# Performance work log

Measured on AMD Instinct MI355X. Metric: run time of the kernel, lower is better.

The kernel has to match this reference:

```python
import jax, jax.numpy as jnp
import numpy as np

N_DIM = 1024   # nodes (rows of s, rows of Kweight)
IN_DIM = 1024  # nodes / feature dim (cols of s, rows of Qweight, side of Gmat)
H_DIM = 64
B = 16


def setup_inputs() -> dict:
    key = jax.random.key(0)
    k1, k2, k3, k4 = jax.random.split(key, 4)
    s = jax.random.normal(k1, (N_DIM, B, IN_DIM), dtype=jnp.float32)
    Gmat = jax.random.uniform(k2, (IN_DIM, IN_DIM), dtype=jnp.float32)
    # torch init: rand * (4/d)**0.5 - (1/d)**0.5  => U[-(1/d)**0.5, (1/d)**0.5]... kept faithful
    Qweight = jax.random.uniform(k3, (IN_DIM, H_DIM), dtype=jnp.float32) * (4.0 / IN_DIM) ** 0.5 - (1.0 / IN_DIM) ** 0.5
    Kweight = jax.random.uniform(k4, (N_DIM, H_DIM), dtype=jnp.float32) * (4.0 / N_DIM) ** 0.5 - (1.0 / N_DIM) ** 0.5
    return {"s": s, "Gmat": Gmat, "Qweight": Qweight, "Kweight": Kweight}


def reference(s, Gmat, Qweight, Kweight):
    h_dim = Qweight.shape[1]
    inv_sqrt_h = 1.0 / jnp.sqrt(jnp.float32(h_dim))
    # q: einsum('ijk,km->ijm', s, Qw).permute(1,0,2) -> (B, n, h)
    q = jnp.einsum('nbi,ih->bnh', s, Qweight)
    # k: s.permute(1,2,0) einsum Kw then permute(0,2,1) -> (B, h, i)
    k = jnp.einsum('nbi,nh->bhi', s, Kweight)
    # squared (non-softmax) attention scores: (B, n, i)
    att = jnp.square(jnp.einsum('bnh,bhi->bni', q, k) * inv_sqrt_h + 1e-9)
    # adjacency aggregation: (B, n, i) @ (i, i)
    att = jnp.einsum('bni,ij->bnj', att, Gmat)
    # row-normalize and permute back to (n, B, i)
    s_t = jnp.sum(att, axis=2, keepdims=True) + 0.001
    return (att / s_t).transpose(1, 0, 2)
```

## Files before the change

### kernel.cpp

```cpp
#include <hip/hip_runtime.h>
#include <hip/hip_bf16.h>
#include <stdint.h>

typedef unsigned short u16;
typedef unsigned int   u32;

#define N_DIM  1024
#define IN_DIM 1024
#define H_DIM  64
#define BATCH  16

typedef __bf16 bf16x8 __attribute__((ext_vector_type(8)));
typedef float  f32x4  __attribute__((ext_vector_type(4)));

__device__ inline u16 f2bf(float f) {
    union { float f; u32 u; } v; v.f = f;
    u32 u = v.u;
    return (u16)((u + 0x7fffu + ((u >> 16) & 1u)) >> 16);
}
__device__ inline u32 pack2(float a, float b) {
    __hip_bfloat162 h = __float22bfloat162_rn(float2{a, b});
    union { __hip_bfloat162 h; u32 u; } cv; cv.h = h; return cv.u;
}

__device__ inline void gl_lds16(const u16* g, u16* l) {
    __builtin_amdgcn_global_load_lds(
        (const __attribute__((address_space(1))) u32*)g,
        (__attribute__((address_space(3))) u32*)l, 16, 0, 0);
}

__global__ __launch_bounds__(256) void prep(
        const float* __restrict__ G, const float* __restrict__ Q,
        const float* __restrict__ Kw, u16* __restrict__ Gbt,
        float* __restrict__ Grp, u16* __restrict__ QT, u16* __restrict__ KwT) {
    int bid = blockIdx.x;
    if (bid >= 256) {
        int idx = (bid - 256) * 256 + threadIdx.x;
        const float* src = (idx < 65536) ? Q : Kw;
        u16* dst = (idx < 65536) ? QT : KwT;
        int i = idx & 65535;
        int h = i >> 10;
        int n = i & 1023;
        dst[h * 1024 + n] = f2bf(src[n * 64 + h]);
        return;
    }
    __shared__ float tile[64][65];
    int jt = bid & 15, it = bid >> 4;
    int i0 = it * 64, j0 = jt * 64;
    int tx = threadIdx.x & 63, ty = threadIdx.x >> 6;
    for (int r = 0; r < 16; ++r) {
        int i = ty * 16 + r;
        tile[i][tx] = G[(size_t)(i0 + i) * 1024 + j0 + tx];
    }
    __syncthreads();
    for (int r = 0; r < 16; ++r) {
        int j = ty * 16 + r;
        Gbt[(size_t)(j0 + j) * 1024 + i0 + tx] = f2bf(tile[tx][j]);
    }
    if (ty == 0) {
        float sum = 0.f;
        for (int j = 0; j < 64; ++j) sum += tile[tx][j];
        Grp[jt * 1024 + i0 + tx] = sum;
    }
}

__global__ __launch_bounds__(512, 4) void qkt(
        const float* __restrict__ s, const u16* __restrict__ QT,
        const u16* __restrict__ KwT, const float* __restrict__ Grp,
        u16* __restrict__ qws, u16* __restrict__ ktws, float* __restrict__ Grsum) {
    int b = blockIdx.y;
    int t = threadIdx.x, lane = t & 63, w = t >> 6, quad = lane >> 4, l15 = lane & 15;
    __shared__ __align__(16) u16 sh[2][2][64][34];
    float* red = (float*)sh;

    if (blockIdx.z == 0) {
        if (blockIdx.y == 0 && t < 64) {
            int i = blockIdx.x * 64 + t;
            float g = 0.f;
            for (int jt = 0; jt < 16; ++jt) g += Grp[jt * 1024 + i];
            Grsum[i] = g;
        }
        int n0 = blockIdx.x * 64;
        int wm = (w & 3) * 16;
        int kb = (w >> 2) * 512;
        const float* arow = s + (size_t)(n0 + wm + l15) * (BATCH * IN_DIM)
                              + (size_t)b * IN_DIM + kb + quad * 8;
        const u16* bbase = QT + (size_t)l15 * 1024 + kb + quad * 8;

        f32x4 acc[4] = {};
        float4 A0[3], A1[3];
        bf16x8 Bf[2][4];
        A0[0] = ((const float4*)arow)[0];
        A1[0] = ((const float4*)arow)[1];
        A0[1] = ((const float4*)(arow + 32))[0];
        A1[1] = ((const float4*)(arow + 32))[1];
#pragma unroll
        for (int ct = 0; ct < 4; ++ct)
            Bf[0][ct] = *(const bf16x8*)&bbase[ct * 16384];

#pragma unroll
        for (int st = 0; st < 16; ++st) {
            int cur = st % 3, cb = st & 1;
            if (st < 14) {
                const float4* ap = (const float4*)(arow + (size_t)(st + 2) * 32);
                A0[(st + 2) % 3] = ap[0];
                A1[(st + 2) % 3] = ap[1];
            }
            if (st < 15) {
#pragma unroll
                for (int ct = 0; ct < 4; ++ct)
                    Bf[cb ^ 1][ct] = *(const bf16x8*)&bbase[ct * 16384 + (st + 1) * 32];
            }
            float4 fa = A0[cur], fb = A1[cur];
            union { uint4 u; bf16x8 v; } cu;
            cu.u = (uint4){ pack2(fa.x, fa.y), pack2(fa.z, fa.w),
                            pack2(fb.x, fb.y), pack2(fb.z, fb.w) };
#pragma unroll
            for (int ct = 0; ct < 4; ++ct)
                acc[ct] = __builtin_amdgcn_mfma_f32_16x16x32_bf16(cu.v, Bf[cb][ct], acc[ct], 0, 0, 0);
        }

        if (w >= 4) {
            float* dst = red + ((w - 4) * 64 + lane) * 16;
#pragma unroll
            for (int ct = 0; ct < 4; ++ct) *(f32x4*)&dst[ct * 4] = acc[ct];
        }
        __syncthreads();
        if (w < 4) {
            const float* sp2 = red + (w * 64 + lane) * 16;
            u16* ob = qws + (size_t)b * 65536;
#pragma unroll
            for (int ct = 0; ct < 4; ++ct) {
                f32x4 o = *(const f32x4*)&sp2[ct * 4];
#pragma unroll
                for (int r = 0; r < 4; ++r) {
                    int m = n0 + wm + quad * 4 + r;
                    ob[(size_t)m * 64 + ct * 16 + l15] = f2bf(acc[ct][r] + o[r]);
                }
            }
        }
        return;
    }

    int i0 = blockIdx.x * 64;
    int half = w >> 2;
    int wm = (w & 3) * 16;
    int shalf = t >> 8, nr = (t & 255) >> 3, iofs = (t & 7) * 8;
    const float* sp = s + (size_t)(shalf * 512 + nr) * (BATCH * IN_DIM)
                        + (size_t)b * IN_DIM + i0 + iofs;
    const u16* bbase = KwT + (size_t)l15 * 1024 + half * 512 + quad * 8;

    f32x4 acc[4] = {};
    float4 P0[2], P1[2];
    bf16x8 Bf[2][4];
    P0[0] = ((const float4*)sp)[0];
    P1[0] = ((const float4*)sp)[1];
    {
        const float4* p = (const float4*)(sp + (size_t)32 * 16384);
        P0[1] = p[0]; P1[1] = p[1];
    }
#pragma unroll
    for (int ct = 0; ct < 4; ++ct)
        Bf[0][ct] = *(const bf16x8*)&bbase[ct * 16384];

#pragma unroll
    for (int c = 0; c < 16; ++c) {
        int buf = c & 1;
        float4 fa = P0[buf], fb = P1[buf];
        u16* wp = &sh[shalf][buf][iofs][nr];
        wp[0]   = f2bf(fa.x);
        wp[34]  = f2bf(fa.y);
        wp[68]  = f2bf(fa.z);
        wp[102] = f2bf(fa.w);
        wp[136] = f2bf(fb.x);
        wp[170] = f2bf(fb.y);
        wp[204] = f2bf(fb.z);
        wp[238] = f2bf(fb.w);
        __syncthreads();
        if (c < 14) {
            const float4* p = (const float4*)(sp + (size_t)(c + 2) * 32 * 16384);
            P0[buf] = p[0]; P1[buf] = p[1];
        }
        if (c < 15) {
#pragma unroll
            for (int ct = 0; ct < 4; ++ct)
                Bf[(c + 1) & 1][ct] = *(const bf16x8*)&bbase[ct * 16384 + (c + 1) * 32];
        }
        const u32* ap = (const u32*)&sh[half][buf][wm + l15][quad * 8];
        union { u32 u[4]; bf16x8 v; } au;
        au.u[0] = ap[0]; au.u[1] = ap[1]; au.u[2] = ap[2]; au.u[3] = ap[3];
#pragma unroll
        for (int ct = 0; ct < 4; ++ct)
            acc[ct] = __builtin_amdgcn_mfma_f32_16x16x32_bf16(au.v, Bf[buf][ct], acc[ct], 0, 0, 0);
    }

    __syncthreads();
    if (w >= 4) {
        float* dst = red + ((w - 4) * 64 + lane) * 16;
#pragma unroll
        for (int ct = 0; ct < 4; ++ct) *(f32x4*)&dst[ct * 4] = acc[ct];
    }
    __syncthreads();
    if (w < 4) {
        const float* sp2 = red + (w * 64 + lane) * 16;
        u16* ob = ktws + (size_t)b * 65536;
#pragma unroll
        for (int ct = 0; ct < 4; ++ct) {
            f32x4 o = *(const f32x4*)&sp2[ct * 4];
#pragma unroll
            for (int r = 0; r < 4; ++r) {
                int i = i0 + wm + quad * 4 + r;
                ob[(size_t)i * 64 + ct * 16 + l15] = f2bf(acc[ct][r] + o[r]);
            }
        }
    }
}

__global__ __launch_bounds__(256, 2) void gemm_fused(
        const u16* __restrict__ qws, const u16* __restrict__ ktws,
        const u16* __restrict__ Gbt, const float* __restrict__ Grsum,
        float* __restrict__ out) {
    int b = blockIdx.z;
    int n0 = blockIdx.x * 256, m0 = blockIdx.y * 128;
    const u16* qb = qws  + (size_t)b * 65536;
    const u16* kb = ktws + (size_t)b * 65536;
    __shared__ __align__(16) u16 As[128 * 40];
    __shared__ __align__(16) u16 Bs[2][256 * 32];
    __shared__ __align__(16) u16 ktc[32 * 72];
    __shared__ __align__(16) float Grs[1024];
    __shared__ float rs[128];
    int t = threadIdx.x, lane = t & 63, w = t >> 6, quad = lane >> 4, l15 = lane & 15;
    int ti = w & 1;
    int wm = (w >> 1) * 64;
    int wn = (w & 1) * 128;

    ((float4*)Grs)[t] = ((const float4*)Grsum)[t];
    if (t < 128) rs[t] = 0.f;

    bf16x8 qf[4][2];
    for (int j = 0; j < 4; ++j)
        for (int kick = 0; kick < 2; ++kick)
            qf[j][kick] = *(const bf16x8*)&qb[(size_t)(m0 + wm + j*16 + l15) * 64 + kick*32 + quad*8];

    int br = t >> 2, bc = ((t & 3) ^ (br & 3)) * 8;
    for (int g4 = 0; g4 < 4; ++g4)
        gl_lds16(Gbt + (size_t)(n0 + br + g4*64) * 1024 + bc, &Bs[0][(br + g4*64) * 32 + (t & 3) * 8]);
    int ir = t >> 3, ch = (t & 7) * 8;
    uint4 kreg = *(const uint4*)&kb[(size_t)ir * 64 + ch];
    int khs = (quad ^ (l15 & 3)) * 8;

    f32x4 acc[4][8] = {};
    float partial[4] = {0.f, 0.f, 0.f, 0.f};

    for (int kk = 0; kk < 32; ++kk) {
        int buf = kk & 1;
        *(uint4*)&ktc[ir * 72 + ch] = kreg;
        __syncthreads();
        f32x4 sacc[4] = {};
        for (int kick = 0; kick < 2; ++kick) {
            bf16x8 ktf = *(const bf16x8*)&ktc[(ti*16 + l15) * 72 + kick*32 + quad*8];
            for (int j = 0; j < 4; ++j)
                sacc[j] = __builtin_amdgcn_mfma_f32_16x16x32_bf16(ktf, qf[j][kick], sacc[j], 0, 0, 0);
        }
        if (kk < 31)
            kreg = *(const uint4*)&kb[(size_t)((kk + 1) * 32 + ir) * 64 + ch];
        float4 g = *(const float4*)&Grs[kk * 32 + ti * 16 + quad * 4];
        for (int j = 0; j < 4; ++j) {
            float v0 = sacc[j][0] * 0.125f + 1e-9f; v0 *= v0;
            float v1 = sacc[j][1] * 0.125f + 1e-9f; v1 *= v1;
            float v2 = sacc[j][2] * 0.125f + 1e-9f; v2 *= v2;
            float v3 = sacc[j][3] * 0.125f + 1e-9f; v3 *= v3;
            partial[j] += v0 * g.x + v1 * g.y + v2 * g.z + v3 * g.w;
            uint2 pk = { pack2(v0, v1), pack2(v2, v3) };
            *(uint2*)&As[(wm + j*16 + l15) * 40 + ti*16 + quad*4] = pk;
        }
        __syncthreads();
        if (kk < 31) {
            for (int g4 = 0; g4 < 4; ++g4)
                gl_lds16(Gbt + (size_t)(n0 + br + g4*64) * 1024 + (kk+1)*32 + bc,
                         &Bs[buf^1][(br + g4*64) * 32 + (t & 3) * 8]);
        }
        int kh = quad * 8;
        bf16x8 af[4];
        for (int i = 0; i < 4; ++i) af[i] = *(const bf16x8*)&As[(wm + i*16 + l15) * 40 + kh];
        for (int jh = 0; jh < 2; ++jh) {
            bf16x8 bfr[4];
            for (int j = 0; j < 4; ++j)
                bfr[j] = *(const bf16x8*)&Bs[buf][(wn + jh*64 + j*16 + l15) * 32 + khs];
            for (int i = 0; i < 4; ++i)
                for (int j = 0; j < 4; ++j)
                    acc[i][jh*4 + j] = __builtin_amdgcn_mfma_f32_16x16x32_bf16(af[i], bfr[j], acc[i][jh*4 + j], 0, 0, 0);
        }
    }

    for (int j = 0; j < 4; ++j) {
        partial[j] += __shfl_xor(partial[j], 16, 64);
        partial[j] += __shfl_xor(partial[j], 32, 64);
    }
    if (quad == 0)
        for (int j = 0; j < 4; ++j) atomicAdd(&rs[wm + j*16 + l15], partial[j]);
    __syncthreads();
    if (t < 128) rs[t] = 1.0f / (rs[t] + 0.001f);
    __syncthreads();

    for (int i = 0; i < 4; ++i) {
        float4 rv = *(const float4*)&rs[wm + i * 16 + quad * 4];
        float rva[4] = { rv.x, rv.y, rv.z, rv.w };
        for (int r = 0; r < 4; ++r) {
            int m = m0 + wm + i * 16 + quad * 4 + r;
            float* orow = out + (size_t)m * (BATCH * IN_DIM) + (size_t)b * IN_DIM + n0 + wn;
            for (int j = 0; j < 8; ++j)
                orow[j * 16 + l15] = acc[i][j][r] * rva[r];
        }
    }
}

extern "C" void kernel_launch(void* const* d_in, const int* in_sizes, int n_in,
                              void* d_out, int out_size, void* d_ws, size_t ws_size,
                              hipStream_t stream) {
    const float* s  = (const float*)d_in[0];
    const float* G  = (const float*)d_in[1];
    const float* Q  = (const float*)d_in[2];
    const float* Kw = (const float*)d_in[3];
    float* out = (float*)d_out;
    char* ws = (char*)d_ws;

    u16*   qws   = (u16*)(ws);
    u16*   ktws  = (u16*)(ws + (size_t)(2u << 20));
    u16*   Gbt   = (u16*)(ws + (size_t)(4u << 20));
    u16*   QT    = (u16*)(ws + (size_t)(6u << 20));
    u16*   KwT   = (u16*)(ws + (size_t)(6u << 20) + (128u << 10));
    float* Grsum = (float*)(ws + (size_t)(6u << 20) + (256u << 10));
    float* Grp   = (float*)(ws + (size_t)(6u << 20) + (260u << 10));

    prep<<<768, 256, 0, stream>>>(G, Q, Kw, Gbt, Grp, QT, KwT);
    qkt<<<dim3(16, 16, 2), 512, 0, stream>>>(s, QT, KwT, Grp, qws, ktws, Grsum);
    gemm_fused<<<dim3(4, 8, 16), 256, 0, stream>>>(qws, ktws, Gbt, Grsum, out);
}
```

Before: 197.5 us.

## Give each warp full-width row tiles and compute its scores independently

```diff
diff --git a/kernel.cpp b/kernel.cpp
--- a/kernel.cpp
+++ b/kernel.cpp
@@ -226,91 +226,113 @@
     const u16* kb = ktws + (size_t)b * 65536;
     __shared__ __align__(16) u16 As[128 * 40];
     __shared__ __align__(16) u16 Bs[2][256 * 32];
-    __shared__ __align__(16) u16 ktc[32 * 72];
     __shared__ __align__(16) float Grs[1024];
-    __shared__ float rs[128];
+    __shared__ float rsw[128];
     int t = threadIdx.x, lane = t & 63, w = t >> 6, quad = lane >> 4, l15 = lane & 15;
-    int ti = w & 1;
-    int wm = (w >> 1) * 64;
-    int wn = (w & 1) * 128;
+    int wm = w * 32;
 
     ((float4*)Grs)[t] = ((const float4*)Grsum)[t];
-    if (t < 128) rs[t] = 0.f;
-
-    bf16x8 qf[4][2];
-    for (int j = 0; j < 4; ++j)
+
+    bf16x8 qf[2][2];
+#pragma unroll
+    for (int jm = 0; jm < 2; ++jm)
+#pragma unroll
         for (int kick = 0; kick < 2; ++kick)
-            qf[j][kick] = *(const bf16x8*)&qb[(size_t)(m0 + wm + j*16 + l15) * 64 + kick*32 + quad*8];
-
-    int br = t >> 2, bc = ((t & 3) ^ (br & 3)) * 8;
+            qf[jm][kick] = *(const bf16x8*)&qb[(size_t)(m0 + wm + jm*16 + l15) * 64 + kick*32 + quad*8];
+
+    int br = t >> 2, bc = (t & 3) * 8;
+#pragma unroll
     for (int g4 = 0; g4 < 4; ++g4)
-        gl_lds16(Gbt + (size_t)(n0 + br + g4*64) * 1024 + bc, &Bs[0][(br + g4*64) * 32 + (t & 3) * 8]);
-    int ir = t >> 3, ch = (t & 7) * 8;
-    uint4 kreg = *(const uint4*)&kb[(size_t)ir * 64 + ch];
-    int khs = (quad ^ (l15 & 3)) * 8;
-
-    f32x4 acc[4][8] = {};
-    float partial[4] = {0.f, 0.f, 0.f, 0.f};
+        gl_lds16(Gbt + (size_t)(n0 + br + g4*64) * 1024 + bc, &Bs[0][(br + g4*64) * 32 + bc]);
+
+    bf16x8 kc[2][2], kn[2][2];
+#pragma unroll
+    for (int it = 0; it < 2; ++it)
+#pragma unroll
+        for (int kick = 0; kick < 2; ++kick)
+            kc[it][kick] = *(const bf16x8*)&kb[(size_t)(it*16 + l15) * 64 + kick*32 + quad*8];
+
+    f32x4 acc[2][16] = {};
+    float partial[2] = {0.f, 0.f};
 
     for (int kk = 0; kk < 32; ++kk) {
         int buf = kk & 1;
-        *(uint4*)&ktc[ir * 72 + ch] = kreg;
-        __syncthreads();
-        f32x4 sacc[4] = {};
-        for (int kick = 0; kick < 2; ++kick) {
-            bf16x8 ktf = *(const bf16x8*)&ktc[(ti*16 + l15) * 72 + kick*32 + quad*8];
-            for (int j = 0; j < 4; ++j)
-                sacc[j] = __builtin_amdgcn_mfma_f32_16x16x32_bf16(ktf, qf[j][kick], sacc[j], 0, 0, 0);
-        }
-        if (kk < 31)
-            kreg = *(const uint4*)&kb[(size_t)((kk + 1) * 32 + ir) * 64 + ch];
-        float4 g = *(const float4*)&Grs[kk * 32 + ti * 16 + quad * 4];
-        for (int j = 0; j < 4; ++j) {
-            float v0 = sacc[j][0] * 0.125f + 1e-9f; v0 *= v0;
-            float v1 = sacc[j][1] * 0.125f + 1e-9f; v1 *= v1;
-            float v2 = sacc[j][2] * 0.125f + 1e-9f; v2 *= v2;
-            float v3 = sacc[j][3] * 0.125f + 1e-9f; v3 *= v3;
-            partial[j] += v0 * g.x + v1 * g.y + v2 * g.z + v3 * g.w;
-            uint2 pk = { pack2(v0, v1), pack2(v2, v3) };
-            *(uint2*)&As[(wm + j*16 + l15) * 40 + ti*16 + quad*4] = pk;
-        }
         __syncthreads();
         if (kk < 31) {
+#pragma unroll
             for (int g4 = 0; g4 < 4; ++g4)
                 gl_lds16(Gbt + (size_t)(n0 + br + g4*64) * 1024 + (kk+1)*32 + bc,
-                         &Bs[buf^1][(br + g4*64) * 32 + (t & 3) * 8]);
-        }
-        int kh = quad * 8;
-        bf16x8 af[4];
-        for (int i = 0; i < 4; ++i) af[i] = *(const bf16x8*)&As[(wm + i*16 + l15) * 40 + kh];
-        for (int jh = 0; jh < 2; ++jh) {
-            bf16x8 bfr[4];
-            for (int j = 0; j < 4; ++j)
-                bfr[j] = *(const bf16x8*)&Bs[buf][(wn + jh*64 + j*16 + l15) * 32 + khs];
-            for (int i = 0; i < 4; ++i)
-                for (int j = 0; j < 4; ++j)
-                    acc[i][jh*4 + j] = __builtin_amdgcn_mfma_f32_16x16x32_bf16(af[i], bfr[j], acc[i][jh*4 + j], 0, 0, 0);
-        }
-    }
-
-    for (int j = 0; j < 4; ++j) {
-        partial[j] += __shfl_xor(partial[j], 16, 64);
-        partial[j] += __shfl_xor(partial[j], 32, 64);
+                         &Bs[buf^1][(br + g4*64) * 32 + bc]);
+        }
+        f32x4 sacc[2][2] = {};
+#pragma unroll
+        for (int kick = 0; kick < 2; ++kick)
+#pragma unroll
+            for (int it = 0; it < 2; ++it)
+#pragma unroll
+                for (int jm = 0; jm < 2; ++jm)
+                    sacc[it][jm] = __builtin_amdgcn_mfma_f32_16x16x32_bf16(
+                        kc[it][kick], qf[jm][kick], sacc[it][jm], 0, 0, 0);
+        if (kk < 31) {
+#pragma unroll
+            for (int it = 0; it < 2; ++it)
+#pragma unroll
+                for (int kick = 0; kick < 2; ++kick)
+                    kn[it][kick] = *(const bf16x8*)&kb[(size_t)((kk+1)*32 + it*16 + l15) * 64 + kick*32 + quad*8];
+        }
+#pragma unroll
+        for (int it = 0; it < 2; ++it) {
+            float4 g = *(const float4*)&Grs[kk * 32 + it * 16 + quad * 4];
+#pragma unroll
+            for (int jm = 0; jm < 2; ++jm) {
+                float v0 = sacc[it][jm][0] * 0.125f + 1e-9f; v0 *= v0;
+                float v1 = sacc[it][jm][1] * 0.125f + 1e-9f; v1 *= v1;
+                float v2 = sacc[it][jm][2] * 0.125f + 1e-9f; v2 *= v2;
+                float v3 = sacc[it][jm][3] * 0.125f + 1e-9f; v3 *= v3;
+                partial[jm] += v0 * g.x + v1 * g.y + v2 * g.z + v3 * g.w;
+                uint2 pk = { pack2(v0, v1), pack2(v2, v3) };
+                *(uint2*)&As[(wm + jm*16 + l15) * 40 + it*16 + quad*4] = pk;
+            }
+        }
+        bf16x8 af[2];
+#pragma unroll
+        for (int mf = 0; mf < 2; ++mf)
+            af[mf] = *(const bf16x8*)&As[(wm + mf*16 + l15) * 40 + quad*8];
+#pragma unroll
+        for (int nf = 0; nf < 16; ++nf) {
+            bf16x8 bfr = *(const bf16x8*)&Bs[buf][(nf*16 + l15) * 32 + quad*8];
+#pragma unroll
+            for (int mf = 0; mf < 2; ++mf)
+                acc[mf][nf] = __builtin_amdgcn_mfma_f32_16x16x32_bf16(af[mf], bfr, acc[mf][nf], 0, 0, 0);
+        }
+#pragma unroll
+        for (int it = 0; it < 2; ++it)
+#pragma unroll
+            for (int kick = 0; kick < 2; ++kick)
+                kc[it][kick] = kn[it][kick];
+    }
+
+#pragma unroll
+    for (int jm = 0; jm < 2; ++jm) {
+        partial[jm] += __shfl_xor(partial[jm], 16, 64);
+        partial[jm] += __shfl_xor(partial[jm], 32, 64);
     }
     if (quad == 0)
-        for (int j = 0; j < 4; ++j) atomicAdd(&rs[wm + j*16 + l15], partial[j]);
-    __syncthreads();
-    if (t < 128) rs[t] = 1.0f / (rs[t] + 0.001f);
-    __syncthreads();
-
-    for (int i = 0; i < 4; ++i) {
-        float4 rv = *(const float4*)&rs[wm + i * 16 + quad * 4];
+#pragma unroll
+        for (int jm = 0; jm < 2; ++jm)
+            rsw[wm + jm*16 + l15] = 1.0f / (partial[jm] + 0.001f);
+
+#pragma unroll
+    for (int mf = 0; mf < 2; ++mf) {
+        float4 rv = *(const float4*)&rsw[wm + mf * 16 + quad * 4];
         float rva[4] = { rv.x, rv.y, rv.z, rv.w };
+#pragma unroll
         for (int r = 0; r < 4; ++r) {
-            int m = m0 + wm + i * 16 + quad * 4 + r;
-            float* orow = out + (size_t)m * (BATCH * IN_DIM) + (size_t)b * IN_DIM + n0 + wn;
-            for (int j = 0; j < 8; ++j)
-                orow[j * 16 + l15] = acc[i][j][r] * rva[r];
+            int m = m0 + wm + mf * 16 + quad * 4 + r;
+            float* orow = out + (size_t)m * (BATCH * IN_DIM) + (size_t)b * IN_DIM + n0;
+#pragma unroll
+            for (int nf = 0; nf < 16; ++nf)
+                orow[nf * 16 + l15] = acc[mf][nf][r] * rva[r];
         }
     }
 }
```

Result: slower. 207.3 us (+5.0%).

## Retile fused GEMM to 64x256 blocks with direct-from-global operand fragments

Applied to the files above, without the earlier changes.

```diff
diff --git a/kernel.cpp b/kernel.cpp
--- a/kernel.cpp
+++ b/kernel.cpp
@@ -21,12 +21,6 @@
 __device__ inline u32 pack2(float a, float b) {
     __hip_bfloat162 h = __float22bfloat162_rn(float2{a, b});
     union { __hip_bfloat162 h; u32 u; } cv; cv.h = h; return cv.u;
-}
-
-__device__ inline void gl_lds16(const u16* g, u16* l) {
-    __builtin_amdgcn_global_load_lds(
-        (const __attribute__((address_space(1))) u32*)g,
-        (__attribute__((address_space(3))) u32*)l, 16, 0, 0);
 }
 
 __global__ __launch_bounds__(256) void prep(
@@ -216,101 +210,87 @@
     }
 }
 
-__global__ __launch_bounds__(256, 2) void gemm_fused(
+__global__ __launch_bounds__(512, 4) void gemm_fused(
         const u16* __restrict__ qws, const u16* __restrict__ ktws,
         const u16* __restrict__ Gbt, const float* __restrict__ Grsum,
         float* __restrict__ out) {
     int b = blockIdx.z;
-    int n0 = blockIdx.x * 256, m0 = blockIdx.y * 128;
+    int n0 = blockIdx.x * 256, m0 = blockIdx.y * 64;
     const u16* qb = qws  + (size_t)b * 65536;
     const u16* kb = ktws + (size_t)b * 65536;
-    __shared__ __align__(16) u16 As[128 * 40];
-    __shared__ __align__(16) u16 Bs[2][256 * 32];
-    __shared__ __align__(16) u16 ktc[32 * 72];
-    __shared__ __align__(16) float Grs[1024];
-    __shared__ float rs[128];
+    __shared__ __align__(16) u16 As[2][64 * 40];
+    __shared__ float rs[64];
     int t = threadIdx.x, lane = t & 63, w = t >> 6, quad = lane >> 4, l15 = lane & 15;
     int ti = w & 1;
-    int wm = (w >> 1) * 64;
-    int wn = (w & 1) * 128;
-
-    ((float4*)Grs)[t] = ((const float4*)Grsum)[t];
-    if (t < 128) rs[t] = 0.f;
-
-    bf16x8 qf[4][2];
-    for (int j = 0; j < 4; ++j)
-        for (int kick = 0; kick < 2; ++kick)
-            qf[j][kick] = *(const bf16x8*)&qb[(size_t)(m0 + wm + j*16 + l15) * 64 + kick*32 + quad*8];
-
-    int br = t >> 2, bc = ((t & 3) ^ (br & 3)) * 8;
-    for (int g4 = 0; g4 < 4; ++g4)
-        gl_lds16(Gbt + (size_t)(n0 + br + g4*64) * 1024 + bc, &Bs[0][(br + g4*64) * 32 + (t & 3) * 8]);
-    int ir = t >> 3, ch = (t & 7) * 8;
-    uint4 kreg = *(const uint4*)&kb[(size_t)ir * 64 + ch];
-    int khs = (quad ^ (l15 & 3)) * 8;
-
-    f32x4 acc[4][8] = {};
-    float partial[4] = {0.f, 0.f, 0.f, 0.f};
+    int sm = (w >> 1) * 16;
+    int wn = w * 32;
+
+    if (t < 64) rs[t] = 0.f;
+
+    bf16x8 qf[2];
+#pragma unroll
+    for (int kick = 0; kick < 2; ++kick)
+        qf[kick] = *(const bf16x8*)&qb[(size_t)(m0 + sm + l15) * 64 + kick*32 + quad*8];
+
+    bf16x8 kc[2], kn[2];
+#pragma unroll
+    for (int kick = 0; kick < 2; ++kick)
+        kc[kick] = *(const bf16x8*)&kb[(size_t)(ti*16 + l15) * 64 + kick*32 + quad*8];
+
+    f32x4 acc[4][2] = {};
+    float partial = 0.f;
 
     for (int kk = 0; kk < 32; ++kk) {
         int buf = kk & 1;
-        *(uint4*)&ktc[ir * 72 + ch] = kreg;
+        bf16x8 gb[2];
+#pragma unroll
+        for (int nf = 0; nf < 2; ++nf)
+            gb[nf] = *(const bf16x8*)&Gbt[(size_t)(n0 + wn + nf*16 + l15) * 1024 + kk*32 + quad*8];
+        if (kk < 31) {
+#pragma unroll
+            for (int kick = 0; kick < 2; ++kick)
+                kn[kick] = *(const bf16x8*)&kb[(size_t)((kk+1)*32 + ti*16 + l15) * 64 + kick*32 + quad*8];
+        }
+        f32x4 sacc = {};
+#pragma unroll
+        for (int kick = 0; kick < 2; ++kick)
+            sacc = __builtin_amdgcn_mfma_f32_16x16x32_bf16(kc[kick], qf[kick], sacc, 0, 0, 0);
+        float4 g = *(const float4*)&Grsum[kk * 32 + ti * 16 + quad * 4];
+        float v0 = sacc[0] * 0.125f + 1e-9f; v0 *= v0;
+        float v1 = sacc[1] * 0.125f + 1e-9f; v1 *= v1;
+        float v2 = sacc[2] * 0.125f + 1e-9f; v2 *= v2;
+        float v3 = sacc[3] * 0.125f + 1e-9f; v3 *= v3;
+        partial += v0 * g.x + v1 * g.y + v2 * g.z + v3 * g.w;
+        uint2 pk = { pack2(v0, v1), pack2(v2, v3) };
+        *(uint2*)&As[buf][(sm + l15) * 40 + ti*16 + quad*4] = pk;
         __syncthreads();
-        f32x4 sacc[4] = {};
-        for (int kick = 0; kick < 2; ++kick) {
-            bf16x8 ktf = *(const bf16x8*)&ktc[(ti*16 + l15) * 72 + kick*32 + quad*8];
-            for (int j = 0; j < 4; ++j)
-                sacc[j] = __builtin_amdgcn_mfma_f32_16x16x32_bf16(ktf, qf[j][kick], sacc[j], 0, 0, 0);
-        }
-        if (kk < 31)
-            kreg = *(const uint4*)&kb[(size_t)((kk + 1) * 32 + ir) * 64 + ch];
-        float4 g = *(const float4*)&Grs[kk * 32 + ti * 16 + quad * 4];
-        for (int j = 0; j < 4; ++j) {
-            float v0 = sacc[j][0] * 0.125f + 1e-9f; v0 *= v0;
-            float v1 = sacc[j][1] * 0.125f + 1e-9f; v1 *= v1;
-            float v2 = sacc[j][2] * 0.125f + 1e-9f; v2 *= v2;
-            float v3 = sacc[j][3] * 0.125f + 1e-9f; v3 *= v3;
-            partial[j] += v0 * g.x + v1 * g.y + v2 * g.z + v3 * g.w;
-            uint2 pk = { pack2(v0, v1), pack2(v2, v3) };
-            *(uint2*)&As[(wm + j*16 + l15) * 40 + ti*16 + quad*4] = pk;
-        }
-        __syncthreads();
-        if (kk < 31) {
-            for (int g4 = 0; g4 < 4; ++g4)
-                gl_lds16(Gbt + (size_t)(n0 + br + g4*64) * 1024 + (kk+1)*32 + bc,
-                         &Bs[buf^1][(br + g4*64) * 32 + (t & 3) * 8]);
-        }
-        int kh = quad * 8;
-        bf16x8 af[4];
-        for (int i = 0; i < 4; ++i) af[i] = *(const bf16x8*)&As[(wm + i*16 + l15) * 40 + kh];
-        for (int jh = 0; jh < 2; ++jh) {
-            bf16x8 bfr[4];
-            for (int j = 0; j < 4; ++j)
-                bfr[j] = *(const bf16x8*)&Bs[buf][(wn + jh*64 + j*16 + l15) * 32 + khs];
-            for (int i = 0; i < 4; ++i)
-                for (int j = 0; j < 4; ++j)
-                    acc[i][jh*4 + j] = __builtin_amdgcn_mfma_f32_16x16x32_bf16(af[i], bfr[j], acc[i][jh*4 + j], 0, 0, 0);
-        }
-    }
-
-    for (int j = 0; j < 4; ++j) {
-        partial[j] += __shfl_xor(partial[j], 16, 64);
-        partial[j] += __shfl_xor(partial[j], 32, 64);
-    }
-    if (quad == 0)
-        for (int j = 0; j < 4; ++j) atomicAdd(&rs[wm + j*16 + l15], partial[j]);
-    __syncthreads();
-    if (t < 128) rs[t] = 1.0f / (rs[t] + 0.001f);
-    __syncthreads();
-
-    for (int i = 0; i < 4; ++i) {
-        float4 rv = *(const float4*)&rs[wm + i * 16 + quad * 4];
+#pragma unroll
+        for (int mf = 0; mf < 4; ++mf) {
+            bf16x8 af = *(const bf16x8*)&As[buf][(mf*16 + l15) * 40 + quad*8];
+            acc[mf][0] = __builtin_amdgcn_mfma_f32_16x16x32_bf16(af, gb[0], acc[mf][0], 0, 0, 0);
+            acc[mf][1] = __builtin_amdgcn_mfma_f32_16x16x32_bf16(af, gb[1], acc[mf][1], 0, 0, 0);
+        }
+        kc[0] = kn[0]; kc[1] = kn[1];
+    }
+
+    partial += __shfl_xor(partial, 16, 64);
+    partial += __shfl_xor(partial, 32, 64);
+    if (quad == 0) atomicAdd(&rs[sm + l15], partial);
+    __syncthreads();
+    if (t < 64) rs[t] = 1.0f / (rs[t] + 0.001f);
+    __syncthreads();
+
+#pragma unroll
+    for (int mf = 0; mf < 4; ++mf) {
+        float4 rv = *(const float4*)&rs[mf * 16 + quad * 4];
         float rva[4] = { rv.x, rv.y, rv.z, rv.w };
+#pragma unroll
         for (int r = 0; r < 4; ++r) {
-            int m = m0 + wm + i * 16 + quad * 4 + r;
+            int m = m0 + mf * 16 + quad * 4 + r;
             float* orow = out + (size_t)m * (BATCH * IN_DIM) + (size_t)b * IN_DIM + n0 + wn;
-            for (int j = 0; j < 8; ++j)
-                orow[j * 16 + l15] = acc[i][j][r] * rva[r];
+#pragma unroll
+            for (int nf = 0; nf < 2; ++nf)
+                orow[nf * 16 + l15] = acc[mf][nf][r] * rva[r];
         }
     }
 }
@@ -335,5 +315,5 @@
 
     prep<<<768, 256, 0, stream>>>(G, Q, Kw, Gbt, Grp, QT, KwT);
     qkt<<<dim3(16, 16, 2), 512, 0, stream>>>(s, QT, KwT, Grp, qws, ktws, Grsum);
-    gemm_fused<<<dim3(4, 8, 16), 256, 0, stream>>>(qws, ktws, Gbt, Grsum, out);
-}
+    gemm_fused<<<dim3(4, 16, 16), 512, 0, stream>>>(qws, ktws, Gbt, Grsum, out);
+}
```

After: 271.2 us. 37.3% more time.

## Software-pipeline score and aggregation stages with one barrier per iteration

Applied to the files above, without the earlier changes.

```diff
diff --git a/kernel.cpp b/kernel.cpp
--- a/kernel.cpp
+++ b/kernel.cpp
@@ -224,91 +224,116 @@
     int n0 = blockIdx.x * 256, m0 = blockIdx.y * 128;
     const u16* qb = qws  + (size_t)b * 65536;
     const u16* kb = ktws + (size_t)b * 65536;
-    __shared__ __align__(16) u16 As[128 * 40];
-    __shared__ __align__(16) u16 Bs[2][256 * 32];
-    __shared__ __align__(16) u16 ktc[32 * 72];
-    __shared__ __align__(16) float Grs[1024];
+    __shared__ __align__(16) u16 As[2][128 * 40];
+    __shared__ __align__(16) u16 Bs[3][256 * 32];
+    __shared__ __align__(16) u16 ktc[2][32 * 68];
     __shared__ float rs[128];
     int t = threadIdx.x, lane = t & 63, w = t >> 6, quad = lane >> 4, l15 = lane & 15;
     int ti = w & 1;
     int wm = (w >> 1) * 64;
     int wn = (w & 1) * 128;
 
-    ((float4*)Grs)[t] = ((const float4*)Grsum)[t];
     if (t < 128) rs[t] = 0.f;
 
     bf16x8 qf[4][2];
+#pragma unroll
     for (int j = 0; j < 4; ++j)
+#pragma unroll
         for (int kick = 0; kick < 2; ++kick)
             qf[j][kick] = *(const bf16x8*)&qb[(size_t)(m0 + wm + j*16 + l15) * 64 + kick*32 + quad*8];
 
-    int br = t >> 2, bc = ((t & 3) ^ (br & 3)) * 8;
+    int br = t >> 2, bc = (t & 3) * 8;
+#pragma unroll
     for (int g4 = 0; g4 < 4; ++g4)
-        gl_lds16(Gbt + (size_t)(n0 + br + g4*64) * 1024 + bc, &Bs[0][(br + g4*64) * 32 + (t & 3) * 8]);
+        gl_lds16(Gbt + (size_t)(n0 + br + g4*64) * 1024 + bc, &Bs[0][(br + g4*64) * 32 + bc]);
     int ir = t >> 3, ch = (t & 7) * 8;
-    uint4 kreg = *(const uint4*)&kb[(size_t)ir * 64 + ch];
-    int khs = (quad ^ (l15 & 3)) * 8;
+    {
+        uint4 k0 = *(const uint4*)&kb[(size_t)ir * 64 + ch];
+        *(uint4*)&ktc[0][ir * 68 + ch] = k0;
+    }
 
     f32x4 acc[4][8] = {};
     float partial[4] = {0.f, 0.f, 0.f, 0.f};
 
-    for (int kk = 0; kk < 32; ++kk) {
-        int buf = kk & 1;
-        *(uint4*)&ktc[ir * 72 + ch] = kreg;
-        __syncthreads();
-        f32x4 sacc[4] = {};
-        for (int kick = 0; kick < 2; ++kick) {
-            bf16x8 ktf = *(const bf16x8*)&ktc[(ti*16 + l15) * 72 + kick*32 + quad*8];
-            for (int j = 0; j < 4; ++j)
-                sacc[j] = __builtin_amdgcn_mfma_f32_16x16x32_bf16(ktf, qf[j][kick], sacc[j], 0, 0, 0);
-        }
-        if (kk < 31)
-            kreg = *(const uint4*)&kb[(size_t)((kk + 1) * 32 + ir) * 64 + ch];
-        float4 g = *(const float4*)&Grs[kk * 32 + ti * 16 + quad * 4];
-        for (int j = 0; j < 4; ++j) {
-            float v0 = sacc[j][0] * 0.125f + 1e-9f; v0 *= v0;
-            float v1 = sacc[j][1] * 0.125f + 1e-9f; v1 *= v1;
-            float v2 = sacc[j][2] * 0.125f + 1e-9f; v2 *= v2;
-            float v3 = sacc[j][3] * 0.125f + 1e-9f; v3 *= v3;
-            partial[j] += v0 * g.x + v1 * g.y + v2 * g.z + v3 * g.w;
-            uint2 pk = { pack2(v0, v1), pack2(v2, v3) };
-            *(uint2*)&As[(wm + j*16 + l15) * 40 + ti*16 + quad*4] = pk;
-        }
+    for (int kk = 0; kk <= 32; ++kk) {
+        int sb = kk & 1;
         __syncthreads();
         if (kk < 31) {
+            int dst = (kk + 1) % 3;
+#pragma unroll
             for (int g4 = 0; g4 < 4; ++g4)
                 gl_lds16(Gbt + (size_t)(n0 + br + g4*64) * 1024 + (kk+1)*32 + bc,
-                         &Bs[buf^1][(br + g4*64) * 32 + (t & 3) * 8]);
-        }
-        int kh = quad * 8;
-        bf16x8 af[4];
-        for (int i = 0; i < 4; ++i) af[i] = *(const bf16x8*)&As[(wm + i*16 + l15) * 40 + kh];
-        for (int jh = 0; jh < 2; ++jh) {
-            bf16x8 bfr[4];
-            for (int j = 0; j < 4; ++j)
-                bfr[j] = *(const bf16x8*)&Bs[buf][(wn + jh*64 + j*16 + l15) * 32 + khs];
+                         &Bs[dst][(br + g4*64) * 32 + bc]);
+        }
+        uint4 kregn;
+        if (kk < 31)
+            kregn = *(const uint4*)&kb[(size_t)((kk + 1) * 32 + ir) * 64 + ch];
+        if (kk < 32) {
+            f32x4 sacc[4] = {};
+#pragma unroll
+            for (int kick = 0; kick < 2; ++kick) {
+                bf16x8 ktf = *(const bf16x8*)&ktc[sb][(ti*16 + l15) * 68 + kick*32 + quad*8];
+#pragma unroll
+                for (int j = 0; j < 4; ++j)
+                    sacc[j] = __builtin_amdgcn_mfma_f32_16x16x32_bf16(ktf, qf[j][kick], sacc[j], 0, 0, 0);
+            }
+            float4 g = *(const float4*)&Grsum[kk * 32 + ti * 16 + quad * 4];
+#pragma unroll
+            for (int j = 0; j < 4; ++j) {
+                float v0 = sacc[j][0] * 0.125f + 1e-9f; v0 *= v0;
+                float v1 = sacc[j][1] * 0.125f + 1e-9f; v1 *= v1;
+                float v2 = sacc[j][2] * 0.125f + 1e-9f; v2 *= v2;
+                float v3 = sacc[j][3] * 0.125f + 1e-9f; v3 *= v3;
+                partial[j] += v0 * g.x + v1 * g.y + v2 * g.z + v3 * g.w;
+                uint2 pk = { pack2(v0, v1), pack2(v2, v3) };
+                *(uint2*)&As[sb][(wm + j*16 + l15) * 40 + ti*16 + quad*4] = pk;
+            }
+        }
+        if (kk > 0) {
+            int bb = (kk - 1) % 3;
+            int kh = quad * 8;
+            bf16x8 af[4];
+#pragma unroll
             for (int i = 0; i < 4; ++i)
+                af[i] = *(const bf16x8*)&As[sb ^ 1][(wm + i*16 + l15) * 40 + kh];
+#pragma unroll
+            for (int jh = 0; jh < 2; ++jh) {
+                bf16x8 bfr[4];
+#pragma unroll
                 for (int j = 0; j < 4; ++j)
-                    acc[i][jh*4 + j] = __builtin_amdgcn_mfma_f32_16x16x32_bf16(af[i], bfr[j], acc[i][jh*4 + j], 0, 0, 0);
-        }
-    }
-
+                    bfr[j] = *(const bf16x8*)&Bs[bb][(wn + jh*64 + j*16 + l15) * 32 + kh];
+#pragma unroll
+                for (int i = 0; i < 4; ++i)
+#pragma unroll
+                    for (int j = 0; j < 4; ++j)
+                        acc[i][jh*4 + j] = __builtin_amdgcn_mfma_f32_16x16x32_bf16(af[i], bfr[j], acc[i][jh*4 + j], 0, 0, 0);
+            }
+        }
+        if (kk < 31)
+            *(uint4*)&ktc[sb ^ 1][ir * 68 + ch] = kregn;
+    }
+
+#pragma unroll
     for (int j = 0; j < 4; ++j) {
         partial[j] += __shfl_xor(partial[j], 16, 64);
         partial[j] += __shfl_xor(partial[j], 32, 64);
     }
     if (quad == 0)
+#pragma unroll
         for (int j = 0; j < 4; ++j) atomicAdd(&rs[wm + j*16 + l15], partial[j]);
     __syncthreads();
     if (t < 128) rs[t] = 1.0f / (rs[t] + 0.001f);
     __syncthreads();
 
+#pragma unroll
     for (int i = 0; i < 4; ++i) {
         float4 rv = *(const float4*)&rs[wm + i * 16 + quad * 4];
         float rva[4] = { rv.x, rv.y, rv.z, rv.w };
+#pragma unroll
         for (int r = 0; r < 4; ++r) {
             int m = m0 + wm + i * 16 + quad * 4 + r;
             float* orow = out + (size_t)m * (BATCH * IN_DIM) + (size_t)b * IN_DIM + n0 + wn;
+#pragma unroll
             for (int j = 0; j < 8; ++j)
                 orow[j * 16 + l15] = acc[i][j][r] * rva[r];
         }
```

Result: faster. 192.7 us (-2.4%).
